# Kernel tuning notes

Measured on AMD Instinct MI355X. Metric: run time of the kernel, lower is better.

The kernel has to match this reference:

```python
import jax, jax.numpy as jnp
import numpy as np

N = 1_000_000
F = 128
B = 4096


def setup_inputs() -> dict:
    key = jax.random.key(0)
    ks = jax.random.split(key, 10)
    x = jax.random.normal(ks[0], (N, F), dtype=jnp.float32)
    E = jax.random.normal(ks[1], (B,), dtype=jnp.float32)
    batch_seg = jnp.sort(jax.random.randint(ks[2], (N,), 0, B)).astype(jnp.int64)
    # params
    Wq = jax.random.normal(ks[3], (F, F), dtype=jnp.float32) / np.sqrt(F)
    bq = jnp.zeros((F,), dtype=jnp.float32)
    Wk = jax.random.normal(ks[4], (F, 2), dtype=jnp.float32)
    Wv = jax.random.normal(ks[5], (F, 2), dtype=jnp.float32)
    # residual MLP (num_residual=1, bias=False)
    W1 = jax.random.normal(ks[6], (F, F), dtype=jnp.float32) / np.sqrt(F)
    W2 = jax.random.normal(ks[7], (F, F), dtype=jnp.float32) / np.sqrt(F)
    return {"x": x, "E": E, "num_batch": B, "batch_seg": batch_seg,
            "Wq": Wq, "bq": bq, "Wk": Wk, "Wv": Wv, "W1": W1, "W2": W2}


def reference(x, E, num_batch, batch_seg, Wq, bq, Wk, Wv, W1, W2):
    eps = 1e-8
    q = x @ Wq.T + bq                                   # [N, F]
    e = jax.nn.relu(jnp.stack([E, -E], axis=-1))        # [B, 2]
    enorm = jnp.maximum(e, jnp.ones_like(e))
    k = ((e / enorm) @ Wk.T)[batch_seg]                 # [N, F] gather
    v = (e @ Wv.T)[batch_seg]                           # [N, F] gather
    dot = jnp.sum(k * q, axis=-1) / jnp.sqrt(jnp.float32(F))  # [N]
    a = jax.nn.softplus(dot)
    anorm = jax.ops.segment_sum(a, batch_seg, num_segments=num_batch)  # [B]
    attn = (a / (anorm[batch_seg] + eps))[:, None]      # [N, 1]
    h = attn * v                                        # [N, F]
    # ResidualMLP, 1 block, bias=False: h = h + W2(silu(W1(silu(h))))
    res = jax.nn.silu(jax.nn.silu(h) @ W1.T) @ W2.T
    return h + res
```

## Files before the change

### kernel.cpp

```cpp
#include <hip/hip_runtime.h>

constexpr int kN = 1000000;
constexpr int kF = 128;
constexpr int kB = 4096;

using short8 = __attribute__((ext_vector_type(8))) short;
using f32x4 = __attribute__((ext_vector_type(4))) float;

__device__ __forceinline__ unsigned short to_bf16(float f) {
  unsigned int u = __builtin_bit_cast(unsigned int, f);
  u += 0x7fffu + ((u >> 16) & 1u);
  return (unsigned short)(u >> 16);
}

__device__ __forceinline__ unsigned int cvt_pk_bf16(float lo, float hi) {
  unsigned int r;
  asm("v_cvt_pk_bf16_f32 %0, %1, %2" : "=v"(r) : "v"(lo), "v"(hi));
  return r;
}

__device__ __forceinline__ float silu_f(float z) {
  return z / (1.f + __expf(-z));
}

__global__ __launch_bounds__(128) void k_precompute(
    const float* __restrict__ E, const float* __restrict__ Wq,
    const float* __restrict__ bq, const float* __restrict__ Wk,
    const float* __restrict__ Wv, float* __restrict__ u,
    float* __restrict__ v, float* __restrict__ cb,
    float* __restrict__ anorm) {
  __shared__ float ksh[kF];
  const int b = blockIdx.x;
  const int f = threadIdx.x;
  const float Eb = E[b];
  const float e0 = fmaxf(Eb, 0.f);
  const float e1 = fmaxf(-Eb, 0.f);
  const float en0 = e0 / fmaxf(e0, 1.f);
  const float en1 = e1 / fmaxf(e1, 1.f);
  const float kf = Wk[2 * f + 0] * en0 + Wk[2 * f + 1] * en1;
  const float vf = Wv[2 * f + 0] * e0 + Wv[2 * f + 1] * e1;
  v[b * kF + f] = vf;
  ksh[f] = kf;
  __syncthreads();
  float uj = 0.f;
#pragma unroll 8
  for (int ff = 0; ff < kF; ++ff) uj = fmaf(Wq[ff * kF + f], ksh[ff], uj);
  u[b * kF + f] = uj;
  if (f == 0) {
    float c = 0.f;
    for (int ff = 0; ff < kF; ++ff) c = fmaf(bq[ff], ksh[ff], c);
    cb[b] = c;
    anorm[b] = 0.f;
  }
}

__global__ __launch_bounds__(256) void k_pass1(
    const float* __restrict__ x, const int* __restrict__ seg,
    const float* __restrict__ u, const float* __restrict__ cb,
    float* __restrict__ a, float* __restrict__ anorm) {
  const int lane = threadIdx.x & 63;
  const int g = lane >> 4;
  const int c = lane & 15;
  const int wave = (int)((blockIdx.x * blockDim.x + threadIdx.x) >> 6);
  const int nw = (int)((gridDim.x * blockDim.x) >> 6);
  const int cpw = (((kN + nw - 1) / nw) + 15) & ~15;
  const int r0 = wave * cpw;
  const int r1 = min(kN, r0 + cpw);
  int bacc = -1;
  float ssum = 0.f;
  for (int rb = r0; rb < r1; rb += 16) {
    float4 xa[4], xb[4], ua[4], ub[4];
    int b4[4];
#pragma unroll
    for (int q = 0; q < 4; ++q) {
      const int row = rb + 4 * q + g;
      const int b = seg[row];
      b4[q] = b;
      const float* xr = x + (size_t)row * kF + c * 8;
      const float* ur = u + (size_t)b * kF + c * 8;
      xa[q] = *reinterpret_cast<const float4*>(xr);
      xb[q] = *reinterpret_cast<const float4*>(xr + 4);
      ua[q] = *reinterpret_cast<const float4*>(ur);
      ub[q] = *reinterpret_cast<const float4*>(ur + 4);
    }
    float av4[4];
#pragma unroll
    for (int q = 0; q < 4; ++q) {
      float p = xa[q].x * ua[q].x;
      p = fmaf(xa[q].y, ua[q].y, p);
      p = fmaf(xa[q].z, ua[q].z, p);
      p = fmaf(xa[q].w, ua[q].w, p);
      p = fmaf(xb[q].x, ub[q].x, p);
      p = fmaf(xb[q].y, ub[q].y, p);
      p = fmaf(xb[q].z, ub[q].z, p);
      p = fmaf(xb[q].w, ub[q].w, p);
#pragma unroll
      for (int o = 1; o < 16; o <<= 1) p += __shfl_xor(p, o);
      const float dot = (p + cb[b4[q]]) * 0.08838834764831845f;
      const float av = fmaxf(dot, 0.f) + __logf(1.f + __expf(-fabsf(dot)));
      av4[q] = av;
      if (c == 0) a[rb + 4 * q + g] = av;
    }
    if (c == 0) {
#pragma unroll
      for (int q = 0; q < 4; ++q) {
        if (b4[q] != bacc) {
          if (bacc >= 0) atomicAdd(anorm + bacc, ssum);
          bacc = b4[q];
          ssum = 0.f;
        }
        ssum += av4[q];
      }
    }
  }
  if (c == 0 && bacc >= 0) atomicAdd(anorm + bacc, ssum);
}

constexpr int kWaves = 8;
constexpr int kStg = 40;

__global__ __launch_bounds__(512) void k_pass2(
    const int* __restrict__ seg, const float* __restrict__ a,
    const float* __restrict__ anorm, const float* __restrict__ v,
    const float* __restrict__ W1, const float* __restrict__ W2,
    float* __restrict__ out) {
  __shared__ __align__(16) unsigned short Wf[2 * 16384];
  __shared__ __align__(16) unsigned short stg[kWaves][16 * kStg];
  const int tid = threadIdx.x;
  for (int idx = tid; idx < 2 * 16384; idx += 512) {
    const int e = idx & 16383;
    const int i = e & 7;
    const int l = (e >> 3) & 63;
    const int kb = (e >> 9) & 3;
    const int nb = (e >> 11) & 7;
    const int cc = l & 15;
    const int col = kb * 32 + ((l >> 4) & 3) * 8 + i;
    const int row = (nb >> 1) * 32 + 2 * cc + (nb & 1);
    const float w = ((idx >> 14) ? W2 : W1)[row * kF + col];
    Wf[idx] = to_bf16(w);
  }
  __syncthreads();

  const int wid = tid >> 6;
  const int lane = tid & 63;
  const int c = lane & 15;
  const int g = lane >> 4;
  unsigned short* __restrict__ st = stg[wid];

  const int gw = blockIdx.x * kWaves + wid;
  const int nw = gridDim.x * kWaves;
  const int niter = kN / 32;

  for (int it = gw; it < niter; it += nw) {
    const int rbase = it * 32;
    const int blo = seg[rbase];
    const int bhi = seg[rbase + 31];
    const bool uni = (blo == bhi);

    int bb[2];
    float attn[2];
    short8 t1[2][4];
    float2 vep[4];

    if (uni) {
      const float an = anorm[blo] + 1e-8f;
      const float* vrow = v + (size_t)blo * kF;
      float4 va[4], vb[4];
#pragma unroll
      for (int kb = 0; kb < 4; ++kb) {
        const int k0 = kb * 32 + g * 8;
        va[kb] = *reinterpret_cast<const float4*>(vrow + k0);
        vb[kb] = *reinterpret_cast<const float4*>(vrow + k0 + 4);
      }
#pragma unroll
      for (int q = 0; q < 4; ++q)
        vep[q] = *reinterpret_cast<const float2*>(vrow + q * 32 + 2 * c);
#pragma unroll
      for (int mt = 0; mt < 2; ++mt) {
        const int row = rbase + mt * 16 + c;
        const float at = a[row] / an;
        attn[mt] = at;
        bb[mt] = blo;
#pragma unroll
        for (int kb = 0; kb < 4; ++kb) {
          uint4 pk;
          pk.x = cvt_pk_bf16(silu_f(at * va[kb].x), silu_f(at * va[kb].y));
          pk.y = cvt_pk_bf16(silu_f(at * va[kb].z), silu_f(at * va[kb].w));
          pk.z = cvt_pk_bf16(silu_f(at * vb[kb].x), silu_f(at * vb[kb].y));
          pk.w = cvt_pk_bf16(silu_f(at * vb[kb].z), silu_f(at * vb[kb].w));
          t1[mt][kb] = __builtin_bit_cast(short8, pk);
        }
      }
    } else {
#pragma unroll
      for (int mt = 0; mt < 2; ++mt) {
        const int row = rbase + mt * 16 + c;
        const int b = seg[row];
        bb[mt] = b;
        const float at = a[row] / (anorm[b] + 1e-8f);
        attn[mt] = at;
        const float* vrow = v + (size_t)b * kF;
#pragma unroll
        for (int kb = 0; kb < 4; ++kb) {
          const int k0 = kb * 32 + g * 8;
          const float4 va = *reinterpret_cast<const float4*>(vrow + k0);
          const float4 vb = *reinterpret_cast<const float4*>(vrow + k0 + 4);
          uint4 pk;
          pk.x = cvt_pk_bf16(silu_f(at * va.x), silu_f(at * va.y));
          pk.y = cvt_pk_bf16(silu_f(at * va.z), silu_f(at * va.w));
          pk.z = cvt_pk_bf16(silu_f(at * vb.x), silu_f(at * vb.y));
          pk.w = cvt_pk_bf16(silu_f(at * vb.z), silu_f(at * vb.w));
          t1[mt][kb] = __builtin_bit_cast(short8, pk);
        }
      }
    }

    f32x4 acc2[2][8];
#pragma unroll
    for (int mt = 0; mt < 2; ++mt)
#pragma unroll
      for (int jb = 0; jb < 8; ++jb) acc2[mt][jb] = (f32x4){0.f, 0.f, 0.f, 0.f};

    __builtin_amdgcn_s_setprio(1);
#pragma unroll
    for (int p = 0; p < 4; ++p) {
      f32x4 z[2][2];
#pragma unroll
      for (int mt = 0; mt < 2; ++mt)
#pragma unroll
        for (int nb = 0; nb < 2; ++nb) z[mt][nb] = (f32x4){0.f, 0.f, 0.f, 0.f};
#pragma unroll
      for (int kb = 0; kb < 4; ++kb) {
        const short8 w0 = *reinterpret_cast<const short8*>(
            &Wf[(((2 * p + 0) * 4 + kb) * 64 + lane) * 8]);
        const short8 w1 = *reinterpret_cast<const short8*>(
            &Wf[(((2 * p + 1) * 4 + kb) * 64 + lane) * 8]);
        z[0][0] = __builtin_amdgcn_mfma_f32_16x16x32_bf16(t1[0][kb], w0,
                                                          z[0][0], 0, 0, 0);
        z[0][1] = __builtin_amdgcn_mfma_f32_16x16x32_bf16(t1[0][kb], w1,
                                                          z[0][1], 0, 0, 0);
        z[1][0] = __builtin_amdgcn_mfma_f32_16x16x32_bf16(t1[1][kb], w0,
                                                          z[1][0], 0, 0, 0);
        z[1][1] = __builtin_amdgcn_mfma_f32_16x16x32_bf16(t1[1][kb], w1,
                                                          z[1][1], 0, 0, 0);
      }
      short8 t2f[2];
#pragma unroll
      for (int mt = 0; mt < 2; ++mt) {
#pragma unroll
        for (int r = 0; r < 4; ++r) {
          const unsigned int pk =
              cvt_pk_bf16(silu_f(z[mt][0][r]), silu_f(z[mt][1][r]));
          *reinterpret_cast<unsigned int*>(
              &st[(g * 4 + r) * kStg + 2 * c]) = pk;
        }
        t2f[mt] =
            *reinterpret_cast<const short8*>(&st[c * kStg + g * 8]);
      }
#pragma unroll
      for (int jb = 0; jb < 8; ++jb) {
        const short8 w2f = *reinterpret_cast<const short8*>(
            &Wf[16384 + ((jb * 4 + p) * 64 + lane) * 8]);
        acc2[0][jb] = __builtin_amdgcn_mfma_f32_16x16x32_bf16(t2f[0], w2f,
                                                              acc2[0][jb], 0, 0, 0);
        acc2[1][jb] = __builtin_amdgcn_mfma_f32_16x16x32_bf16(t2f[1], w2f,
                                                              acc2[1][jb], 0, 0, 0);
      }
    }
    __builtin_amdgcn_s_setprio(0);

    if (uni) {
#pragma unroll
      for (int mt = 0; mt < 2; ++mt) {
#pragma unroll
        for (int r = 0; r < 4; ++r) {
          const float at4 = __shfl(attn[mt], g * 4 + r);
          const int row = rbase + mt * 16 + g * 4 + r;
          float* orow = out + (size_t)row * kF;
#pragma unroll
          for (int q = 0; q < 4; ++q) {
            float2 o;
            o.x = fmaf(at4, vep[q].x, acc2[mt][2 * q + 0][r]);
            o.y = fmaf(at4, vep[q].y, acc2[mt][2 * q + 1][r]);
            *reinterpret_cast<float2*>(orow + q * 32 + 2 * c) = o;
          }
        }
      }
    } else {
#pragma unroll
      for (int mt = 0; mt < 2; ++mt) {
#pragma unroll
        for (int r = 0; r < 4; ++r) {
          const int b4 = __shfl(bb[mt], g * 4 + r);
          const float at4 = __shfl(attn[mt], g * 4 + r);
          const float* vr = v + (size_t)b4 * kF;
          const int row = rbase + mt * 16 + g * 4 + r;
          float* orow = out + (size_t)row * kF;
#pragma unroll
          for (int q = 0; q < 4; ++q) {
            const float2 vv =
                *reinterpret_cast<const float2*>(vr + q * 32 + 2 * c);
            float2 o;
            o.x = fmaf(at4, vv.x, acc2[mt][2 * q + 0][r]);
            o.y = fmaf(at4, vv.y, acc2[mt][2 * q + 1][r]);
            *reinterpret_cast<float2*>(orow + q * 32 + 2 * c) = o;
          }
        }
      }
    }
  }
}

extern "C" void kernel_launch(void* const* d_in, const int* in_sizes, int n_in,
                              void* d_out, int out_size, void* d_ws,
                              size_t ws_size, hipStream_t stream) {
  const float* x = (const float*)d_in[0];
  const float* E = (const float*)d_in[1];
  const int* seg = (const int*)d_in[3];
  const float* Wq = (const float*)d_in[4];
  const float* bq = (const float*)d_in[5];
  const float* Wk = (const float*)d_in[6];
  const float* Wv = (const float*)d_in[7];
  const float* W1 = (const float*)d_in[8];
  const float* W2 = (const float*)d_in[9];
  float* out = (float*)d_out;

  float* u = (float*)d_ws;
  float* v = u + (size_t)kB * kF;
  float* cb = v + (size_t)kB * kF;
  float* anorm = cb + kB;
  float* a = anorm + kB;

  k_precompute<<<kB, kF, 0, stream>>>(E, Wq, bq, Wk, Wv, u, v, cb, anorm);
  k_pass1<<<2048, 256, 0, stream>>>(x, seg, u, cb, a, anorm);
  k_pass2<<<512, 512, 0, stream>>>(seg, a, anorm, v, W1, W2, out);
}
```

Before: 360.7 us.

## Move W2 bf16 fragments out of LDS to global memory to raise pass2 occupancy

A new small kernel converts W2 to bf16 in MFMA fragment order and writes it to workspace. k_pass2 now keeps only W1 in shared memory and reads W2 fragments from global memory, which should be cache-resident. This halves the weight LDS footprint so more blocks fit per CU, and the launch grows to 768 blocks with launch bounds asking for 6 blocks. The cost is an extra launch plus global/L2 loads in the inner GEMM loop where LDS reads were used before.

Result: slower. 1.093 ms (+203.0%).

```diff
diff --git a/kernel.cpp b/kernel.cpp
--- a/kernel.cpp
+++ b/kernel.cpp
@@ -21,6 +21,19 @@
 
 __device__ __forceinline__ float silu_f(float z) {
   return z / (1.f + __expf(-z));
+}
+
+__global__ __launch_bounds__(256) void k_prepw(const float* __restrict__ W2,
+                                               unsigned short* __restrict__ w2p) {
+  const int idx = blockIdx.x * 256 + threadIdx.x;
+  const int i = idx & 7;
+  const int l = (idx >> 3) & 63;
+  const int kb = (idx >> 9) & 3;
+  const int nb = (idx >> 11) & 7;
+  const int cc = l & 15;
+  const int col = kb * 32 + ((l >> 4) & 3) * 8 + i;
+  const int row = (nb >> 1) * 32 + 2 * cc + (nb & 1);
+  w2p[idx] = to_bf16(W2[row * kF + col]);
 }
 
 __global__ __launch_bounds__(128) void k_precompute(
@@ -119,25 +132,23 @@
 constexpr int kWaves = 8;
 constexpr int kStg = 40;
 
-__global__ __launch_bounds__(512) void k_pass2(
+__global__ __launch_bounds__(512, 6) void k_pass2(
     const int* __restrict__ seg, const float* __restrict__ a,
     const float* __restrict__ anorm, const float* __restrict__ v,
-    const float* __restrict__ W1, const float* __restrict__ W2,
+    const float* __restrict__ W1, const unsigned short* __restrict__ w2p,
     float* __restrict__ out) {
-  __shared__ __align__(16) unsigned short Wf[2 * 16384];
+  __shared__ __align__(16) unsigned short Wf[16384];
   __shared__ __align__(16) unsigned short stg[kWaves][16 * kStg];
   const int tid = threadIdx.x;
-  for (int idx = tid; idx < 2 * 16384; idx += 512) {
-    const int e = idx & 16383;
-    const int i = e & 7;
-    const int l = (e >> 3) & 63;
-    const int kb = (e >> 9) & 3;
-    const int nb = (e >> 11) & 7;
+  for (int idx = tid; idx < 16384; idx += 512) {
+    const int i = idx & 7;
+    const int l = (idx >> 3) & 63;
+    const int kb = (idx >> 9) & 3;
+    const int nb = (idx >> 11) & 7;
     const int cc = l & 15;
     const int col = kb * 32 + ((l >> 4) & 3) * 8 + i;
     const int row = (nb >> 1) * 32 + 2 * cc + (nb & 1);
-    const float w = ((idx >> 14) ? W2 : W1)[row * kF + col];
-    Wf[idx] = to_bf16(w);
+    Wf[idx] = to_bf16(W1[row * kF + col]);
   }
   __syncthreads();
 
@@ -260,7 +271,7 @@
 #pragma unroll
       for (int jb = 0; jb < 8; ++jb) {
         const short8 w2f = *reinterpret_cast<const short8*>(
-            &Wf[16384 + ((jb * 4 + p) * 64 + lane) * 8]);
+            &w2p[((jb * 4 + p) * 64 + lane) * 8]);
         acc2[0][jb] = __builtin_amdgcn_mfma_f32_16x16x32_bf16(t2f[0], w2f,
                                                               acc2[0][jb], 0, 0, 0);
         acc2[1][jb] = __builtin_amdgcn_mfma_f32_16x16x32_bf16(t2f[1], w2f,
@@ -330,8 +341,10 @@
   float* cb = v + (size_t)kB * kF;
   float* anorm = cb + kB;
   float* a = anorm + kB;
-
+  unsigned short* w2p = (unsigned short*)(a + kN);
+
+  k_prepw<<<64, 256, 0, stream>>>(W2, w2p);
   k_precompute<<<kB, kF, 0, stream>>>(E, Wq, bq, Wk, Wv, u, v, cb, anorm);
   k_pass1<<<2048, 256, 0, stream>>>(x, seg, u, cb, a, anorm);
-  k_pass2<<<512, 512, 0, stream>>>(seg, a, anorm, v, W1, W2, out);
-}
+  k_pass2<<<768, 512, 0, stream>>>(seg, a, anorm, v, W1, w2p, out);
+}
```
